# Optimization experiments

Measured on AMD Instinct MI355X. Metric: run time of the kernel, lower is better.

## Reference

```python
import jax, jax.numpy as jnp
import numpy as np
import math

B, N, C = 8, 4096, 768
H = 12
DH = C // H
M = 256
LN_EPS = 1e-5


def setup_inputs() -> dict:
    key = jax.random.key(0)
    ks = jax.random.split(key, 7)
    x = jax.random.normal(ks[0], (B, N, C), dtype=jnp.float32)
    # torch Linear weight [out,in]; store transposed for y = x @ W
    W_qkv = jax.random.normal(ks[1], (C, 3 * C), dtype=jnp.float32) * (1.0 / math.sqrt(C))
    W_proj = jax.random.normal(ks[2], (C, C), dtype=jnp.float32) * (1.0 / math.sqrt(C))
    b_proj = jnp.zeros((C,), dtype=jnp.float32)
    gamma = jnp.ones((C,), dtype=jnp.float32)
    beta = jnp.zeros((C,), dtype=jnp.float32)
    random_features = jax.random.normal(ks[3], (M, DH), dtype=jnp.float32) / math.sqrt(DH)
    return {"x": x, "W_qkv": W_qkv, "W_proj": W_proj, "b_proj": b_proj,
            "gamma": gamma, "beta": beta, "random_features": random_features}


def _phi(t, random_features):
    # t: [B, H, N, DH] -> [B, H, N, M]; phi(x) = exp(w·x - ||x||^2/2) / sqrt(M)
    norm_sq = 0.5 * jnp.sum(t * t, axis=-1, keepdims=True)
    proj = jnp.einsum('bhnd,md->bhnm', t, random_features)
    return jnp.exp(proj - norm_sq) * (1.0 / math.sqrt(M))


def reference(x, W_qkv, W_proj, b_proj, gamma, beta, random_features):
    b, n, c = x.shape
    qkv = (x @ W_qkv).reshape(b, n, 3, H, DH)
    qkv = jnp.transpose(qkv, (2, 0, 3, 1, 4))  # [3, B, H, N, DH]
    q, k, v = qkv[0], qkv[1], qkv[2]

    q_p = _phi(q, random_features)  # [B,H,N,M]
    k_p = _phi(k, random_features)  # [B,H,N,M]

    kv = jnp.einsum('bhnm,bhnd->bhmd', k_p, v)       # [B,H,M,DH]
    out = jnp.einsum('bhnm,bhmd->bhnd', q_p, kv)     # [B,H,N,DH]

    k_sum = jnp.sum(k_p, axis=2)                      # [B,H,M]
    normalizer = jnp.einsum('bhnm,bhm->bhn', q_p, k_sum)[..., None]
    out = out / (normalizer + 1e-6)

    x_attn = jnp.transpose(out, (0, 2, 1, 3)).reshape(b, n, c)
    x_attn = x_attn @ W_proj + b_proj
    # dropout is identity in eval / p=0

    y = x + x_attn
    mu = jnp.mean(y, axis=-1, keepdims=True)
    var = jnp.mean(jnp.square(y - mu), axis=-1, keepdims=True)
    return (y - mu) * jax.lax.rsqrt(var + LN_EPS) * gamma + beta
```

## Files before the change

kernel.cpp:

```cpp
#include <hip/hip_runtime.h>
#include <hip/hip_fp16.h>


#define LOG2E 1.44269504088896340736f

typedef _Float16 half8 __attribute__((ext_vector_type(8)));
typedef _Float16 half4_t __attribute__((ext_vector_type(4)));
typedef _Float16 half2_t __attribute__((ext_vector_type(2)));
typedef float f32x4 __attribute__((ext_vector_type(4)));

#if __has_builtin(__builtin_amdgcn_fdot2)
#define FDOT2(a, b, c) __builtin_amdgcn_fdot2((a), (b), (c), false)
#else
#define FDOT2(a, b, c) \
  ((float)(a)[0] * (float)(b)[0] + ((float)(a)[1] * (float)(b)[1] + (c)))
#endif

static __device__ __forceinline__ half2_t pk2(float a, float b) {
#if __has_builtin(__builtin_amdgcn_cvt_pkrtz)
  return __builtin_bit_cast(half2_t, __builtin_amdgcn_cvt_pkrtz(a, b));
#else
  half2_t r; r[0] = (_Float16)a; r[1] = (_Float16)b; return r;
#endif
}

__device__ __forceinline__ void glds16(const _Float16* g, _Float16* s) {
  __builtin_amdgcn_global_load_lds(
      (const __attribute__((address_space(1))) void*)g,
      (__attribute__((address_space(3))) unsigned int*)s,
      16, 0, 0);
}


__global__ __launch_bounds__(256)
void prep(const float* __restrict__ x, const float* __restrict__ Wqkv,
          const float* __restrict__ Wproj, const float* __restrict__ rfm,
          _Float16* __restrict__ x_h, _Float16* __restrict__ wqkvT,
          _Float16* __restrict__ wprojT, _Float16* __restrict__ rfh) {
  __shared__ _Float16 T[64][72];
  const int bid = blockIdx.x;
  if (bid < 12288) {
    long i = ((long)bid * 256 + threadIdx.x) * 8;
    float4 v0 = *(const float4*)(x + i);
    float4 v1 = *(const float4*)(x + i + 4);
    half8 h;
    h[0] = (_Float16)v0.x; h[1] = (_Float16)v0.y; h[2] = (_Float16)v0.z; h[3] = (_Float16)v0.w;
    h[4] = (_Float16)v1.x; h[5] = (_Float16)v1.y; h[6] = (_Float16)v1.z; h[7] = (_Float16)v1.w;
    *(half8*)(x_h + i) = h;
    return;
  }
  int tb = bid - 12288;
  if (tb < 576) {
    const float* src; _Float16* dst; int Csrc, r0, c0;
    if (tb < 432) {
      r0 = (tb / 36) * 64; c0 = (tb % 36) * 64; src = Wqkv; dst = wqkvT; Csrc = 2304;
    } else {
      int t2 = tb - 432;
      r0 = (t2 / 12) * 64; c0 = (t2 % 12) * 64; src = Wproj; dst = wprojT; Csrc = 768;
    }
    const int ri = threadIdx.x >> 4;
    const int ci = (threadIdx.x & 15) * 4;
#pragma unroll
    for (int rr = 0; rr < 4; ++rr) {
      float4 v = *(const float4*)(src + (long)(r0 + ri * 4 + rr) * Csrc + c0 + ci);
      T[ci + 0][ri * 4 + rr] = (_Float16)v.x;
      T[ci + 1][ri * 4 + rr] = (_Float16)v.y;
      T[ci + 2][ri * 4 + rr] = (_Float16)v.z;
      T[ci + 3][ri * 4 + rr] = (_Float16)v.w;
    }
    __syncthreads();
    const int wi = threadIdx.x >> 3;
    const int wj = (threadIdx.x & 7) * 8;
#pragma unroll
    for (int ww = 0; ww < 2; ++ww) {
      const int row = wi * 2 + ww;
      half8 h = *(const half8*)(&T[row][wj]);
      *(half8*)(dst + (long)(c0 + row) * 768 + r0 + wj) = h;
    }
  } else {
    int idx = (tb - 576) * 256 + threadIdx.x;
    if (idx < 16384) rfh[idx] = (_Float16)rfm[idx];
  }
}


__device__ __forceinline__ void stage_unit(const _Float16* __restrict__ G, int grow0,
                                           int kcol, _Float16* lds, int w, int l) {
#pragma unroll
  for (int j = 0; j < 2; ++j) {
    const int ci = w + j * 8;
    const int row = ci * 8 + (l >> 3);
    const int col8 = (l & 7) ^ (row & 7);
    glds16(G + (long)(grow0 + row) * 768 + kcol + col8 * 8, lds + ci * 512);
  }
}

static __device__ __forceinline__ half8 ldsw(const _Float16* buf, int r, int sl) {
  return *(const half8*)(buf + r * 64 + ((sl ^ (r & 7)) << 3));
}

__global__ __launch_bounds__(512)
void gemm_qkv(const _Float16* __restrict__ W, const _Float16* __restrict__ X,
              _Float16* __restrict__ qh, _Float16* __restrict__ kh,
              _Float16* __restrict__ vT,
              float* __restrict__ nsqLq, float* __restrict__ nsqLk) {
  __shared__ __align__(16) _Float16 SMEM[65536];
  _Float16* As = SMEM;
  _Float16* Bs = SMEM + 32768;
  const int tid = threadIdx.x;
  const int w = tid >> 6, l = tid & 63;
  const int lr = l & 15, kg = l >> 4;
  const int wr = w >> 2, wc = w & 3;

  const int bid = blockIdx.x;
  const int wg = (bid & 7) * 144 + (bid >> 3);
  const int m0 = (wg % 9) * 256;
  const int n0 = (wg / 9) * 256;

  stage_unit(W, m0,       0,  As,         w, l);
  stage_unit(W, m0 + 128, 0,  As + 8192,  w, l);
  stage_unit(X, n0,       0,  Bs,         w, l);
  stage_unit(X, n0 + 128, 0,  Bs + 8192,  w, l);
  stage_unit(W, m0,       64, As + 16384, w, l);
  stage_unit(X, n0,       64, Bs + 16384, w, l);
  stage_unit(X, n0 + 128, 64, Bs + 24576, w, l);
  asm volatile("s_waitcnt vmcnt(6)" ::: "memory");
  __builtin_amdgcn_s_barrier();

  f32x4 acc[8][4];
#pragma unroll
  for (int t = 0; t < 8; ++t)
#pragma unroll
    for (int u = 0; u < 4; ++u) acc[t][u] = (f32x4){0.f, 0.f, 0.f, 0.f};

  for (int kt = 0; kt < 12; ++kt) {
    const int c = kt & 1, o = c ^ 1;
    const _Float16* Ac = As + c * 16384;
    const _Float16* Bc = Bs + c * 16384;
    half8 a0[4][2], a1[4][2], b0[2][2], b1[2][2];

#pragma unroll
    for (int i = 0; i < 4; ++i) {
      const int r = wr * 16 + i * 32 + lr;
      a0[i][0] = ldsw(Ac, r, kg);
      a0[i][1] = ldsw(Ac, r, 4 + kg);
    }
#pragma unroll
    for (int j = 0; j < 2; ++j) {
      const int r = wc * 16 + j * 64 + lr;
      b0[j][0] = ldsw(Bc, r, kg);
      b0[j][1] = ldsw(Bc, r, 4 + kg);
    }
#pragma unroll
    for (int j = 0; j < 2; ++j) {
      const int r = 128 + wc * 16 + j * 64 + lr;
      b1[j][0] = ldsw(Bc, r, kg);
      b1[j][1] = ldsw(Bc, r, 4 + kg);
    }
#pragma unroll
    for (int i = 0; i < 4; ++i) {
      const int r = 128 + wr * 16 + i * 32 + lr;
      a1[i][0] = ldsw(Ac, r, kg);
      a1[i][1] = ldsw(Ac, r, 4 + kg);
    }
    if (kt + 1 < 12)
      stage_unit(W, m0 + 128, (kt + 1) * 64, As + o * 16384 + 8192, w, l);

    __builtin_amdgcn_s_setprio(1);
#pragma unroll
    for (int ks = 0; ks < 2; ++ks)
#pragma unroll
      for (int i = 0; i < 4; ++i)
#pragma unroll
        for (int j = 0; j < 2; ++j)
          acc[i][j] = __builtin_amdgcn_mfma_f32_16x16x32_f16(a0[i][ks], b0[j][ks],
                                                             acc[i][j], 0, 0, 0);
#pragma unroll
    for (int ks = 0; ks < 2; ++ks)
#pragma unroll
      for (int i = 0; i < 4; ++i)
#pragma unroll
        for (int j = 0; j < 2; ++j)
          acc[i][2 + j] = __builtin_amdgcn_mfma_f32_16x16x32_f16(a0[i][ks], b1[j][ks],
                                                                 acc[i][2 + j], 0, 0, 0);
#pragma unroll
    for (int ks = 0; ks < 2; ++ks)
#pragma unroll
      for (int i = 0; i < 4; ++i)
#pragma unroll
        for (int j = 0; j < 2; ++j)
          acc[4 + i][2 + j] = __builtin_amdgcn_mfma_f32_16x16x32_f16(a1[i][ks], b1[j][ks],
                                                                     acc[4 + i][2 + j], 0, 0, 0);
#pragma unroll
    for (int ks = 0; ks < 2; ++ks)
#pragma unroll
      for (int i = 0; i < 4; ++i)
#pragma unroll
        for (int j = 0; j < 2; ++j)
          acc[4 + i][j] = __builtin_amdgcn_mfma_f32_16x16x32_f16(a1[i][ks], b0[j][ks],
                                                                 acc[4 + i][j], 0, 0, 0);
    __builtin_amdgcn_s_setprio(0);

    __builtin_amdgcn_s_barrier();
    if (kt + 2 < 12) {
      stage_unit(W, m0, (kt + 2) * 64, As + c * 16384, w, l);
      stage_unit(X, n0, (kt + 2) * 64, Bs + c * 16384, w, l);
      stage_unit(X, n0 + 128, (kt + 2) * 64, Bs + c * 16384 + 8192, w, l);
    }
    if (kt < 10)
      asm volatile("s_waitcnt vmcnt(6)" ::: "memory");
    else
      asm volatile("s_waitcnt vmcnt(0)" ::: "memory");
    __builtin_amdgcn_s_barrier();
  }

  const int which = (m0 >= 1536) ? 2 : ((m0 >= 768) ? 1 : 0);
  const int hbase = (m0 - which * 768) >> 6;
  const int b_ = n0 >> 12;
  const int nb = n0 & 4095;

  if (which < 2) {
    _Float16* dst = which ? kh : qh;
    float* nd = which ? nsqLk : nsqLq;
#pragma unroll
    for (int t = 0; t < 8; ++t) {
      const int m_ = wr * 16 + t * 32 + kg * 4;
#pragma unroll
      for (int u = 0; u < 4; ++u) {
        const int n_ = wc * 16 + u * 64 + lr;
        half2_t h01 = pk2(acc[t][u][0], acc[t][u][1]);
        half2_t h23 = pk2(acc[t][u][2], acc[t][u][3]);
        half4_t p4; p4[0] = h01[0]; p4[1] = h01[1]; p4[2] = h23[0]; p4[3] = h23[1];
        *(half4_t*)((char*)SMEM + n_ * 512 + (((m_ >> 3) ^ (n_ & 7)) << 4) +
                    (m_ & 4) * 2) = p4;
      }
    }
    __syncthreads();
    const int h2 = w >> 1;
    const int jj = l & 7;
    const long bhout = (long)(b_ * 12 + hbase + h2);
#pragma unroll
    for (int i = 0; i < 16; ++i) {
      const int n_ = (w & 1) * 128 + i * 8 + (l >> 3);
      const int phys = (h2 * 8 + jj) ^ (n_ & 7);
      half8 v = *(const half8*)((const char*)SMEM + n_ * 512 + phys * 16);
      *(half8*)(dst + (bhout * 4096 + nb + n_) * 64 + jj * 8) = v;
      float s = 0.f;
#pragma unroll
      for (int e = 0; e < 8; ++e) { float f = (float)v[e]; s += f * f; }
      s += __shfl_xor(s, 1);
      s += __shfl_xor(s, 2);
      s += __shfl_xor(s, 4);
      if (jj == 0) nd[bhout * 4096 + nb + n_] = 0.5f * s * LOG2E + 4.0f;
    }
  } else {
#pragma unroll
    for (int t = 0; t < 8; ++t) {
#pragma unroll
      for (int u = 0; u < 4; ++u) {
        const int n_ = wc * 16 + u * 64 + lr;
#pragma unroll
        for (int r = 0; r < 4; ++r) {
          const int m_ = wr * 16 + t * 32 + kg * 4 + r;
          *(_Float16*)((char*)SMEM + m_ * 512 + ((((n_ >> 3)) ^ (m_ & 7)) << 4) +
                       (n_ & 7) * 2) = (_Float16)acc[t][u][r];
        }
      }
    }
    __syncthreads();
#pragma unroll
    for (int i = 0; i < 16; ++i) {
      const int m_ = w * 32 + i * 2 + (l >> 5);
      const int c = l & 31;
      half8 v = *(const half8*)((const char*)SMEM + m_ * 512 + ((c ^ (m_ & 7)) << 4));
      const int h2 = m_ >> 6, d = m_ & 63;
      *(half8*)(vT + ((long)(b_ * 12 + hbase + h2) * 64 + d) * 4096 + nb + c * 8) = v;
    }
  }
}


__global__ __launch_bounds__(512)
void proj_ln(const _Float16* __restrict__ A, const _Float16* __restrict__ BT,
             const float* __restrict__ bias, const float* __restrict__ xres,
             const float* __restrict__ gamma, const float* __restrict__ beta,
             float* __restrict__ y) {
  __shared__ __align__(16) _Float16 Asm[64 * 768];
  __shared__ __align__(16) float lnS[64][8];
  __shared__ __align__(16) float lnQ[64][8];
  const int tid = threadIdx.x;
  const int w = tid >> 6, l = tid & 63;
  const int lr = l & 15, kg = l >> 4;
  const int m0 = blockIdx.x * 64;
  const int ncol0 = w * 96;

#pragma unroll
  for (int i = 0; i < 12; ++i) {
    const int sg = i * 512 + tid;
    const int row = sg / 96;
    const int p = sg - row * 96;
    glds16(A + (long)(m0 + row) * 768 + ((p ^ (row & 7)) << 3), Asm + sg * 8);
  }
  asm volatile("s_waitcnt vmcnt(0)" ::: "memory");
  __builtin_amdgcn_s_barrier();

  f32x4 acc[4][6];
#pragma unroll
  for (int mf = 0; mf < 4; ++mf)
#pragma unroll
    for (int nf = 0; nf < 6; ++nf) acc[mf][nf] = (f32x4){0.f, 0.f, 0.f, 0.f};

#pragma unroll 2
  for (int kc = 0; kc < 12; ++kc) {
    half8 bf[6][2];
#pragma unroll
    for (int nf = 0; nf < 6; ++nf)
#pragma unroll
      for (int ks = 0; ks < 2; ++ks)
        bf[nf][ks] = *(const half8*)(BT + (long)(ncol0 + nf * 16 + lr) * 768 +
                                     kc * 64 + ks * 32 + kg * 8);
    half8 af[4][2];
#pragma unroll
    for (int mf = 0; mf < 4; ++mf) {
      const int r = mf * 16 + lr;
#pragma unroll
      for (int ks = 0; ks < 2; ++ks)
        af[mf][ks] = *(const half8*)(Asm + r * 768 +
                                     (((kc * 8 + ks * 4 + kg) ^ (lr & 7)) << 3));
    }
#pragma unroll
    for (int ks = 0; ks < 2; ++ks)
#pragma unroll
      for (int mf = 0; mf < 4; ++mf)
#pragma unroll
        for (int nf = 0; nf < 6; ++nf)
          acc[mf][nf] = __builtin_amdgcn_mfma_f32_16x16x32_f16(af[mf][ks], bf[nf][ks],
                                                               acc[mf][nf], 0, 0, 0);
  }

  float bv[6], gv[6], betv[6];
#pragma unroll
  for (int nf = 0; nf < 6; ++nf) {
    const int col = ncol0 + nf * 16 + lr;
    bv[nf] = bias[col]; gv[nf] = gamma[col]; betv[nf] = beta[col];
  }
#pragma unroll
  for (int mf = 0; mf < 4; ++mf)
#pragma unroll
    for (int r = 0; r < 4; ++r) {
      const int row = mf * 16 + kg * 4 + r;
#pragma unroll
      for (int nf = 0; nf < 6; ++nf)
        acc[mf][nf][r] += bv[nf] + xres[(long)(m0 + row) * 768 + ncol0 + nf * 16 + lr];
    }
#pragma unroll
  for (int mf = 0; mf < 4; ++mf)
#pragma unroll
    for (int r = 0; r < 4; ++r) {
      float s = 0.f, q = 0.f;
#pragma unroll
      for (int nf = 0; nf < 6; ++nf) {
        const float v = acc[mf][nf][r];
        s += v; q += v * v;
      }
      s += __shfl_xor(s, 1); q += __shfl_xor(q, 1);
      s += __shfl_xor(s, 2); q += __shfl_xor(q, 2);
      s += __shfl_xor(s, 4); q += __shfl_xor(q, 4);
      s += __shfl_xor(s, 8); q += __shfl_xor(q, 8);
      if (lr == 0) {
        const int row = mf * 16 + kg * 4 + r;
        lnS[row][w] = s; lnQ[row][w] = q;
      }
    }
  __syncthreads();
#pragma unroll
  for (int mf = 0; mf < 4; ++mf)
#pragma unroll
    for (int r = 0; r < 4; ++r) {
      const int row = mf * 16 + kg * 4 + r;
      f32x4 s0 = *(const f32x4*)&lnS[row][0];
      f32x4 s1 = *(const f32x4*)&lnS[row][4];
      f32x4 q0 = *(const f32x4*)&lnQ[row][0];
      f32x4 q1 = *(const f32x4*)&lnQ[row][4];
      const float s = s0[0] + s0[1] + s0[2] + s0[3] + s1[0] + s1[1] + s1[2] + s1[3];
      const float q = q0[0] + q0[1] + q0[2] + q0[3] + q1[0] + q1[1] + q1[2] + q1[3];
      const float mu = s * (1.f / 768.f);
      const float var = q * (1.f / 768.f) - mu * mu;
      const float rstd = rsqrtf(var + 1e-5f);
#pragma unroll
      for (int nf = 0; nf < 6; ++nf)
        y[(long)(m0 + row) * 768 + ncol0 + nf * 16 + lr] =
            (acc[mf][nf][r] - mu) * rstd * gv[nf] + betv[nf];
    }
}


__global__ __launch_bounds__(256)
void kv_fused(const _Float16* __restrict__ kh, const _Float16* __restrict__ vT,
              const _Float16* __restrict__ rfh, const float* __restrict__ nsqLk,
              _Float16* __restrict__ kvpart, float* __restrict__ kspart) {
  __shared__ __align__(16) _Float16 P[256 * 72];
  const int chunk = blockIdx.x, bh = blockIdx.y;
  const int tid = threadIdx.x, w = tid >> 6, l = tid & 63;
  const int lr = l & 15, kg = l >> 4;
  const long khbase = (long)bh * 4096 * 64;
  const long vtbase = (long)bh * 64 * 4096;
  const half2_t ONES = {(_Float16)1.f, (_Float16)1.f};

  half8 rf[4][2];
#pragma unroll
  for (int u = 0; u < 4; ++u)
#pragma unroll
    for (int ks = 0; ks < 2; ++ks)
      rf[u][ks] = *(const half8*)(rfh + (w * 64 + u * 16 + lr) * 64 + ks * 32 + kg * 8);

  f32x4 kvacc[4][4];
#pragma unroll
  for (int mt = 0; mt < 4; ++mt)
#pragma unroll
    for (int dt = 0; dt < 4; ++dt) kvacc[mt][dt] = (f32x4){0.f, 0.f, 0.f, 0.f};
  float ksacc[4] = {0.f, 0.f, 0.f, 0.f};

  for (int t8 = 0; t8 < 8; ++t8) {
    const int nt = chunk * 512 + t8 * 64;

    half8 af[4][2];
#pragma unroll
    for (int tt = 0; tt < 4; ++tt)
#pragma unroll
      for (int ks = 0; ks < 2; ++ks)
        af[tt][ks] = *(const half8*)(kh + khbase + (long)(nt + tt * 16 + lr) * 64 +
                                     ks * 32 + kg * 8);

    f32x4 sacc[4][4];
#pragma unroll
    for (int tt = 0; tt < 4; ++tt)
#pragma unroll
      for (int u = 0; u < 4; ++u) sacc[tt][u] = (f32x4){0.f, 0.f, 0.f, 0.f};
#pragma unroll
    for (int ks = 0; ks < 2; ++ks)
#pragma unroll
      for (int tt = 0; tt < 4; ++tt)
#pragma unroll
        for (int u = 0; u < 4; ++u)
          sacc[tt][u] = __builtin_amdgcn_mfma_f32_16x16x32_f16(af[tt][ks], rf[u][ks],
                                                               sacc[tt][u], 0, 0, 0);
    float4 nsq4[4];
#pragma unroll
    for (int tt = 0; tt < 4; ++tt)
      nsq4[tt] = *(const float4*)(nsqLk + (long)bh * 4096 + nt + tt * 16 + kg * 4);
#pragma unroll
    for (int tt = 0; tt < 4; ++tt)
#pragma unroll
      for (int u = 0; u < 4; ++u) {
        float e0 = exp2f(sacc[tt][u][0] * LOG2E - nsq4[tt].x);
        float e1 = exp2f(sacc[tt][u][1] * LOG2E - nsq4[tt].y);
        float e2 = exp2f(sacc[tt][u][2] * LOG2E - nsq4[tt].z);
        float e3 = exp2f(sacc[tt][u][3] * LOG2E - nsq4[tt].w);
        half2_t h01 = pk2(e0, e1), h23 = pk2(e2, e3);
        half4_t p4; p4[0] = h01[0]; p4[1] = h01[1]; p4[2] = h23[0]; p4[3] = h23[1];
        *(half4_t*)(P + (w * 64 + u * 16 + lr) * 72 + tt * 16 + kg * 4) = p4;
      }

#pragma unroll
    for (int ks = 0; ks < 2; ++ks) {
      half8 pa[4], bv[4];
#pragma unroll
      for (int mt = 0; mt < 4; ++mt)
        pa[mt] = *(const half8*)(P + (w * 64 + mt * 16 + lr) * 72 + ks * 32 + kg * 8);
#pragma unroll
      for (int dt = 0; dt < 4; ++dt)
        bv[dt] = *(const half8*)(vT + vtbase + (long)(dt * 16 + lr) * 4096 + nt +
                                 ks * 32 + kg * 8);
#pragma unroll
      for (int mt = 0; mt < 4; ++mt)
#pragma unroll
        for (int dt = 0; dt < 4; ++dt)
          kvacc[mt][dt] = __builtin_amdgcn_mfma_f32_16x16x32_f16(pa[mt], bv[dt],
                                                                 kvacc[mt][dt], 0, 0, 0);
#pragma unroll
      for (int mt = 0; mt < 4; ++mt) {
        const half2_t* pp = (const half2_t*)&pa[mt];
#pragma unroll
        for (int p = 0; p < 4; ++p) ksacc[mt] = FDOT2(pp[p], ONES, ksacc[mt]);
      }
    }
  }

#pragma unroll
  for (int mt = 0; mt < 4; ++mt) {
    float v = ksacc[mt];
    v += __shfl_xor(v, 16);
    v += __shfl_xor(v, 32);
    if (l < 16) kspart[((bh * 8 + chunk) << 8) + w * 64 + mt * 16 + l] = v;
  }
#pragma unroll
  for (int mt = 0; mt < 4; ++mt)
#pragma unroll
    for (int dt = 0; dt < 4; ++dt)
#pragma unroll
      for (int r = 0; r < 4; ++r)
        kvpart[(((long)(bh * 8 + chunk) * 256) + w * 64 + mt * 16 + kg * 4 + r) * 64 +
               dt * 16 + lr] = (_Float16)kvacc[mt][dt][r];
}


__global__ __launch_bounds__(256)
void reduce_all(const _Float16* __restrict__ kvpart, const float* __restrict__ kspart,
                _Float16* __restrict__ kvT, _Float16* __restrict__ ksumh) {
  if (blockIdx.x < 6144) {
    long i = (long)blockIdx.x * 256 + threadIdx.x;
    const int bh = (int)(i >> 14);
    const int rem = (int)(i & 16383);
    const int m = rem >> 6, d = rem & 63;
    float s = 0.f;
#pragma unroll
    for (int c = 0; c < 8; ++c)
      s += (float)kvpart[(((long)bh * 8 + c) * 256 + m) * 64 + d];
    kvT[(long)bh * 16384 + d * 256 + m] = (_Float16)s;
  } else {
    int i = (blockIdx.x - 6144) * 256 + threadIdx.x;
    int bh = i >> 8, m = i & 255;
    float s = 0.f;
#pragma unroll
    for (int c = 0; c < 8; ++c) s += kspart[((bh * 8 + c) << 8) + m];
    ksumh[i] = (_Float16)s;
  }
}


__global__ __launch_bounds__(256)
void attn_fused(const _Float16* __restrict__ qh, const _Float16* __restrict__ rfh,
                const float* __restrict__ nsqLq, const _Float16* __restrict__ kvT,
                const _Float16* __restrict__ ksumh, _Float16* __restrict__ attn) {
  __shared__ __align__(16) _Float16 KV[64 * 264];
  __shared__ __align__(16) _Float16 KS[256];
  __shared__ __align__(16) _Float16 P[64 * 264];
  __shared__ __align__(16) float NS[64];
  const int chunk = blockIdx.x, bh = blockIdx.y;
  const int b = bh / 12, h = bh % 12;
  const int tid = threadIdx.x, w = tid >> 6, l = tid & 63;
  const int lr = l & 15, kg = l >> 4;

  {
    const int d = tid >> 2, mb = (tid & 3) * 64;
#pragma unroll
    for (int j = 0; j < 8; ++j)
      *(half8*)(KV + d * 264 + mb + j * 8) =
          *(const half8*)(kvT + (long)bh * 16384 + d * 256 + mb + j * 8);
    if (tid < 32) *(half8*)(KS + tid * 8) = *(const half8*)(ksumh + bh * 256 + tid * 8);
  }

  half8 rf[4][2];
#pragma unroll
  for (int mt = 0; mt < 4; ++mt)
#pragma unroll
    for (int ks = 0; ks < 2; ++ks)
      rf[mt][ks] = *(const half8*)(rfh + (w * 64 + mt * 16 + lr) * 64 + ks * 32 + kg * 8);

  for (int t8 = 0; t8 < 4; ++t8) {
    const int nt = chunk * 256 + t8 * 64;
    __syncthreads();

    half8 bq[4][2];
#pragma unroll
    for (int tt = 0; tt < 4; ++tt)
#pragma unroll
      for (int ks = 0; ks < 2; ++ks)
        bq[tt][ks] = *(const half8*)(qh + ((long)bh * 4096 + nt + tt * 16 + lr) * 64 +
                                     ks * 32 + kg * 8);

    f32x4 sacc[4][4];
#pragma unroll
    for (int mt = 0; mt < 4; ++mt)
#pragma unroll
      for (int tt = 0; tt < 4; ++tt) sacc[mt][tt] = (f32x4){0.f, 0.f, 0.f, 0.f};
#pragma unroll
    for (int ks = 0; ks < 2; ++ks)
#pragma unroll
      for (int mt = 0; mt < 4; ++mt)
#pragma unroll
        for (int tt = 0; tt < 4; ++tt)
          sacc[mt][tt] = __builtin_amdgcn_mfma_f32_16x16x32_f16(rf[mt][ks], bq[tt][ks],
                                                                sacc[mt][tt], 0, 0, 0);
    float nsqv[4];
#pragma unroll
    for (int tt = 0; tt < 4; ++tt)
      nsqv[tt] = nsqLq[(long)bh * 4096 + nt + tt * 16 + lr];
#pragma unroll
    for (int mt = 0; mt < 4; ++mt)
#pragma unroll
      for (int tt = 0; tt < 4; ++tt) {
        float e0 = exp2f(sacc[mt][tt][0] * LOG2E - nsqv[tt]);
        float e1 = exp2f(sacc[mt][tt][1] * LOG2E - nsqv[tt]);
        float e2 = exp2f(sacc[mt][tt][2] * LOG2E - nsqv[tt]);
        float e3 = exp2f(sacc[mt][tt][3] * LOG2E - nsqv[tt]);
        half2_t h01 = pk2(e0, e1), h23 = pk2(e2, e3);
        half4_t p4; p4[0] = h01[0]; p4[1] = h01[1]; p4[2] = h23[0]; p4[3] = h23[1];
        *(half4_t*)(P + (tt * 16 + lr) * 264 + w * 64 + mt * 16 + kg * 4) = p4;
      }
    __syncthreads();

    f32x4 oacc[4];
#pragma unroll
    for (int u = 0; u < 4; ++u) oacc[u] = (f32x4){0.f, 0.f, 0.f, 0.f};
    float nacc = 0.f;
#pragma unroll
    for (int ks = 0; ks < 8; ++ks) {
      half8 ap = *(const half8*)(P + (w * 16 + lr) * 264 + ks * 32 + kg * 8);
      half8 kv8 = *(const half8*)(KS + ks * 32 + kg * 8);
      const half2_t* a2 = (const half2_t*)&ap;
      const half2_t* k2 = (const half2_t*)&kv8;
#pragma unroll
      for (int p = 0; p < 4; ++p) nacc = FDOT2(a2[p], k2[p], nacc);
#pragma unroll
      for (int u = 0; u < 4; ++u) {
        half8 bkv = *(const half8*)(KV + (u * 16 + lr) * 264 + ks * 32 + kg * 8);
        oacc[u] = __builtin_amdgcn_mfma_f32_16x16x32_f16(ap, bkv, oacc[u], 0, 0, 0);
      }
    }
    nacc += __shfl_xor(nacc, 16);
    nacc += __shfl_xor(nacc, 32);
    if (l < 16) NS[w * 16 + l] = nacc;
    f32x4 n4 = *(const f32x4*)(NS + w * 16 + kg * 4);
    float inv[4];
#pragma unroll
    for (int r = 0; r < 4; ++r) inv[r] = 1.f / (n4[r] + 1e-6f);
#pragma unroll
    for (int u = 0; u < 4; ++u)
#pragma unroll
      for (int r = 0; r < 4; ++r)
        attn[((long)b * 4096 + nt + w * 16 + kg * 4 + r) * 768 + h * 64 + u * 16 + lr] =
            (_Float16)(oacc[u][r] * inv[r]);
  }
}


extern "C" void kernel_launch(void* const* d_in, const int* in_sizes, int n_in,
                              void* d_out, int out_size, void* d_ws, size_t ws_size,
                              hipStream_t stream) {
  const float* x = (const float*)d_in[0];
  const float* Wqkv = (const float*)d_in[1];
  const float* Wproj = (const float*)d_in[2];
  const float* bproj = (const float*)d_in[3];
  const float* gamma = (const float*)d_in[4];
  const float* beta = (const float*)d_in[5];
  const float* rfm = (const float*)d_in[6];

  char* ws = (char*)d_ws;
  size_t off = 0;
  auto alloc = [&](size_t bytes) -> void* {
    void* p = ws + off;
    off += (bytes + 255) & ~(size_t)255;
    return p;
  };
  char* regionA = (char*)alloc(50331648ULL);
  _Float16* x_h = (_Float16*)regionA;
  _Float16* kvpart = (_Float16*)regionA;
  _Float16* attn = (_Float16*)regionA;

  _Float16* wqkvT = (_Float16*)alloc(1769472ULL * 2);
  _Float16* wprojT = (_Float16*)alloc(589824ULL * 2);
  _Float16* rfh = (_Float16*)alloc(16384ULL * 2);
  _Float16* qh = (_Float16*)alloc(25165824ULL * 2);
  _Float16* kh = (_Float16*)alloc(25165824ULL * 2);
  _Float16* vT = (_Float16*)alloc(25165824ULL * 2);
  float* nsqLq = (float*)alloc(393216ULL * 4);
  float* nsqLk = (float*)alloc(393216ULL * 4);
  float* kspart = (float*)alloc(96ULL * 8 * 256 * 4);
  _Float16* kvT = (_Float16*)alloc(96ULL * 16384 * 2);
  _Float16* ksumh = (_Float16*)alloc(96ULL * 256 * 2);

  float* y = (float*)d_out;

  prep<<<12928, 256, 0, stream>>>(x, Wqkv, Wproj, rfm, x_h, wqkvT, wprojT, rfh);
  gemm_qkv<<<1152, 512, 0, stream>>>(wqkvT, x_h, qh, kh, vT, nsqLq, nsqLk);
  kv_fused<<<dim3(8, 96), 256, 0, stream>>>(kh, vT, rfh, nsqLk, kvpart, kspart);
  reduce_all<<<6240, 256, 0, stream>>>(kvpart, kspart, kvT, ksumh);
  attn_fused<<<dim3(16, 96), 256, 0, stream>>>(qh, rfh, nsqLq, kvT, ksumh, attn);
  proj_ln<<<512, 512, 0, stream>>>(attn, wprojT, bproj, x, gamma, beta, y);
}
```

Baseline: 578.1 us.

## Shrink QKV GEMM tile to 128x128 with triple-buffered BK=32 pipeline

The QKV projection GEMM moves from 256x256 tiles with 512 threads and double-buffered K=64 stages to 128x128 tiles with 256 threads and a three-stage ring of K=32 buffers. It uses a new swizzled LDS layout and a lighter epilogue. The goal is higher occupancy, since LDS use drops from 128KB to 48KB per block, and a grid of 4608 blocks for better load balance across CUs. The cost is lower arithmetic intensity per tile, so more global and LDS traffic per FLOP, and more barriers per unit of K.

```diff
diff --git a/kernel.cpp b/kernel.cpp
--- a/kernel.cpp
+++ b/kernel.cpp
@@ -84,134 +84,80 @@
 }
 
 
-__device__ __forceinline__ void stage_unit(const _Float16* __restrict__ G, int grow0,
-                                           int kcol, _Float16* lds, int w, int l) {
+__device__ __forceinline__ void stage32(const _Float16* __restrict__ G, int grow0,
+                                        int kcol, _Float16* lds, int w, int l) {
 #pragma unroll
   for (int j = 0; j < 2; ++j) {
-    const int ci = w + j * 8;
-    const int row = ci * 8 + (l >> 3);
-    const int col8 = (l & 7) ^ (row & 7);
-    glds16(G + (long)(grow0 + row) * 768 + kcol + col8 * 8, lds + ci * 512);
-  }
-}
-
-static __device__ __forceinline__ half8 ldsw(const _Float16* buf, int r, int sl) {
-  return *(const half8*)(buf + r * 64 + ((sl ^ (r & 7)) << 3));
-}
-
-__global__ __launch_bounds__(512)
+    const int ci = w + j * 4;
+    const int p = ci * 8 + (l >> 3);
+    const int tmp = (l & 7) ^ (p & 7);
+    const int r = 2 * p + (tmp >> 2);
+    const int kc = tmp & 3;
+    glds16(G + (long)(grow0 + r) * 768 + kcol + kc * 8, lds + ci * 512);
+  }
+}
+
+static __device__ __forceinline__ half8 ld32(const _Float16* buf, int m, int kg) {
+  return *(const half8*)((const char*)buf + (m >> 1) * 128 +
+                         (((kg + (m & 1) * 4) ^ ((m >> 1) & 7)) << 4));
+}
+
+__global__ __launch_bounds__(256)
 void gemm_qkv(const _Float16* __restrict__ W, const _Float16* __restrict__ X,
               _Float16* __restrict__ qh, _Float16* __restrict__ kh,
               _Float16* __restrict__ vT,
               float* __restrict__ nsqLq, float* __restrict__ nsqLk) {
-  __shared__ __align__(16) _Float16 SMEM[65536];
-  _Float16* As = SMEM;
-  _Float16* Bs = SMEM + 32768;
+  __shared__ __align__(16) _Float16 SMEM[24576];
   const int tid = threadIdx.x;
   const int w = tid >> 6, l = tid & 63;
   const int lr = l & 15, kg = l >> 4;
-  const int wr = w >> 2, wc = w & 3;
+  const int wm = (w >> 1) * 64, wn = (w & 1) * 64;
 
   const int bid = blockIdx.x;
-  const int wg = (bid & 7) * 144 + (bid >> 3);
-  const int m0 = (wg % 9) * 256;
-  const int n0 = (wg / 9) * 256;
-
-  stage_unit(W, m0,       0,  As,         w, l);
-  stage_unit(W, m0 + 128, 0,  As + 8192,  w, l);
-  stage_unit(X, n0,       0,  Bs,         w, l);
-  stage_unit(X, n0 + 128, 0,  Bs + 8192,  w, l);
-  stage_unit(W, m0,       64, As + 16384, w, l);
-  stage_unit(X, n0,       64, Bs + 16384, w, l);
-  stage_unit(X, n0 + 128, 64, Bs + 24576, w, l);
-  asm volatile("s_waitcnt vmcnt(6)" ::: "memory");
+  const int wg = (bid & 7) * 576 + (bid >> 3);
+  const int m0 = (wg % 18) * 128;
+  const int n0 = (wg / 18) * 128;
+
+  stage32(W, m0, 0, SMEM, w, l);
+  stage32(X, n0, 0, SMEM + 4096, w, l);
+  stage32(W, m0, 32, SMEM + 8192, w, l);
+  stage32(X, n0, 32, SMEM + 8192 + 4096, w, l);
+  asm volatile("s_waitcnt vmcnt(4)" ::: "memory");
   __builtin_amdgcn_s_barrier();
 
-  f32x4 acc[8][4];
-#pragma unroll
-  for (int t = 0; t < 8; ++t)
+  f32x4 acc[4][4];
+#pragma unroll
+  for (int t = 0; t < 4; ++t)
 #pragma unroll
     for (int u = 0; u < 4; ++u) acc[t][u] = (f32x4){0.f, 0.f, 0.f, 0.f};
 
-  for (int kt = 0; kt < 12; ++kt) {
-    const int c = kt & 1, o = c ^ 1;
-    const _Float16* Ac = As + c * 16384;
-    const _Float16* Bc = Bs + c * 16384;
-    half8 a0[4][2], a1[4][2], b0[2][2], b1[2][2];
-
-#pragma unroll
-    for (int i = 0; i < 4; ++i) {
-      const int r = wr * 16 + i * 32 + lr;
-      a0[i][0] = ldsw(Ac, r, kg);
-      a0[i][1] = ldsw(Ac, r, 4 + kg);
-    }
-#pragma unroll
-    for (int j = 0; j < 2; ++j) {
-      const int r = wc * 16 + j * 64 + lr;
-      b0[j][0] = ldsw(Bc, r, kg);
-      b0[j][1] = ldsw(Bc, r, 4 + kg);
-    }
-#pragma unroll
-    for (int j = 0; j < 2; ++j) {
-      const int r = 128 + wc * 16 + j * 64 + lr;
-      b1[j][0] = ldsw(Bc, r, kg);
-      b1[j][1] = ldsw(Bc, r, 4 + kg);
-    }
-#pragma unroll
-    for (int i = 0; i < 4; ++i) {
-      const int r = 128 + wr * 16 + i * 32 + lr;
-      a1[i][0] = ldsw(Ac, r, kg);
-      a1[i][1] = ldsw(Ac, r, 4 + kg);
-    }
-    if (kt + 1 < 12)
-      stage_unit(W, m0 + 128, (kt + 1) * 64, As + o * 16384 + 8192, w, l);
-
+  int s = 0, s2 = 2;
+  for (int kt = 0; kt < 24; ++kt) {
+    const _Float16* Ab = SMEM + s * 8192;
+    const _Float16* Bb = Ab + 4096;
+    half8 af[4], bf[4];
+#pragma unroll
+    for (int t = 0; t < 4; ++t) af[t] = ld32(Ab, wm + t * 16 + lr, kg);
+#pragma unroll
+    for (int u = 0; u < 4; ++u) bf[u] = ld32(Bb, wn + u * 16 + lr, kg);
+    if (kt + 2 < 24) {
+      stage32(W, m0, (kt + 2) * 32, SMEM + s2 * 8192, w, l);
+      stage32(X, n0, (kt + 2) * 32, SMEM + s2 * 8192 + 4096, w, l);
+    }
     __builtin_amdgcn_s_setprio(1);
 #pragma unroll
-    for (int ks = 0; ks < 2; ++ks)
-#pragma unroll
-      for (int i = 0; i < 4; ++i)
-#pragma unroll
-        for (int j = 0; j < 2; ++j)
-          acc[i][j] = __builtin_amdgcn_mfma_f32_16x16x32_f16(a0[i][ks], b0[j][ks],
-                                                             acc[i][j], 0, 0, 0);
-#pragma unroll
-    for (int ks = 0; ks < 2; ++ks)
-#pragma unroll
-      for (int i = 0; i < 4; ++i)
-#pragma unroll
-        for (int j = 0; j < 2; ++j)
-          acc[i][2 + j] = __builtin_amdgcn_mfma_f32_16x16x32_f16(a0[i][ks], b1[j][ks],
-                                                                 acc[i][2 + j], 0, 0, 0);
-#pragma unroll
-    for (int ks = 0; ks < 2; ++ks)
-#pragma unroll
-      for (int i = 0; i < 4; ++i)
-#pragma unroll
-        for (int j = 0; j < 2; ++j)
-          acc[4 + i][2 + j] = __builtin_amdgcn_mfma_f32_16x16x32_f16(a1[i][ks], b1[j][ks],
-                                                                     acc[4 + i][2 + j], 0, 0, 0);
-#pragma unroll
-    for (int ks = 0; ks < 2; ++ks)
-#pragma unroll
-      for (int i = 0; i < 4; ++i)
-#pragma unroll
-        for (int j = 0; j < 2; ++j)
-          acc[4 + i][j] = __builtin_amdgcn_mfma_f32_16x16x32_f16(a1[i][ks], b0[j][ks],
-                                                                 acc[4 + i][j], 0, 0, 0);
+    for (int t = 0; t < 4; ++t)
+#pragma unroll
+      for (int u = 0; u < 4; ++u)
+        acc[t][u] = __builtin_amdgcn_mfma_f32_16x16x32_f16(af[t], bf[u], acc[t][u], 0, 0, 0);
     __builtin_amdgcn_s_setprio(0);
-
-    __builtin_amdgcn_s_barrier();
-    if (kt + 2 < 12) {
-      stage_unit(W, m0, (kt + 2) * 64, As + c * 16384, w, l);
-      stage_unit(X, n0, (kt + 2) * 64, Bs + c * 16384, w, l);
-      stage_unit(X, n0 + 128, (kt + 2) * 64, Bs + c * 16384 + 8192, w, l);
-    }
-    if (kt < 10)
-      asm volatile("s_waitcnt vmcnt(6)" ::: "memory");
+    if (kt < 22)
+      asm volatile("s_waitcnt vmcnt(4)" ::: "memory");
     else
       asm volatile("s_waitcnt vmcnt(0)" ::: "memory");
     __builtin_amdgcn_s_barrier();
+    s = (s == 2) ? 0 : s + 1;
+    s2 = (s2 == 2) ? 0 : s2 + 1;
   }
 
   const int which = (m0 >= 1536) ? 2 : ((m0 >= 768) ? 1 : 0);
@@ -223,58 +169,59 @@
     _Float16* dst = which ? kh : qh;
     float* nd = which ? nsqLk : nsqLq;
 #pragma unroll
-    for (int t = 0; t < 8; ++t) {
-      const int m_ = wr * 16 + t * 32 + kg * 4;
+    for (int t = 0; t < 4; ++t) {
+      const int m_ = wm + t * 16 + kg * 4;
 #pragma unroll
       for (int u = 0; u < 4; ++u) {
-        const int n_ = wc * 16 + u * 64 + lr;
+        const int n_ = wn + u * 16 + lr;
         half2_t h01 = pk2(acc[t][u][0], acc[t][u][1]);
         half2_t h23 = pk2(acc[t][u][2], acc[t][u][3]);
         half4_t p4; p4[0] = h01[0]; p4[1] = h01[1]; p4[2] = h23[0]; p4[3] = h23[1];
-        *(half4_t*)((char*)SMEM + n_ * 512 + (((m_ >> 3) ^ (n_ & 7)) << 4) +
+        *(half4_t*)((char*)SMEM + n_ * 256 + (((m_ >> 3) ^ (n_ & 7)) << 4) +
                     (m_ & 4) * 2) = p4;
       }
     }
     __syncthreads();
-    const int h2 = w >> 1;
+    const int h2 = w & 1;
     const int jj = l & 7;
     const long bhout = (long)(b_ * 12 + hbase + h2);
 #pragma unroll
-    for (int i = 0; i < 16; ++i) {
-      const int n_ = (w & 1) * 128 + i * 8 + (l >> 3);
+    for (int i = 0; i < 8; ++i) {
+      const int n_ = (w >> 1) * 64 + i * 8 + (l >> 3);
       const int phys = (h2 * 8 + jj) ^ (n_ & 7);
-      half8 v = *(const half8*)((const char*)SMEM + n_ * 512 + phys * 16);
+      half8 v = *(const half8*)((const char*)SMEM + n_ * 256 + phys * 16);
       *(half8*)(dst + (bhout * 4096 + nb + n_) * 64 + jj * 8) = v;
-      float s = 0.f;
-#pragma unroll
-      for (int e = 0; e < 8; ++e) { float f = (float)v[e]; s += f * f; }
-      s += __shfl_xor(s, 1);
-      s += __shfl_xor(s, 2);
-      s += __shfl_xor(s, 4);
-      if (jj == 0) nd[bhout * 4096 + nb + n_] = 0.5f * s * LOG2E + 4.0f;
+      float sq = 0.f;
+#pragma unroll
+      for (int e = 0; e < 8; ++e) { float f = (float)v[e]; sq += f * f; }
+      sq += __shfl_xor(sq, 1);
+      sq += __shfl_xor(sq, 2);
+      sq += __shfl_xor(sq, 4);
+      if (jj == 0) nd[bhout * 4096 + nb + n_] = 0.5f * sq * LOG2E + 4.0f;
     }
   } else {
 #pragma unroll
-    for (int t = 0; t < 8; ++t) {
+    for (int t = 0; t < 4; ++t) {
 #pragma unroll
       for (int u = 0; u < 4; ++u) {
-        const int n_ = wc * 16 + u * 64 + lr;
+        const int n_ = wn + u * 16 + lr;
 #pragma unroll
         for (int r = 0; r < 4; ++r) {
-          const int m_ = wr * 16 + t * 32 + kg * 4 + r;
-          *(_Float16*)((char*)SMEM + m_ * 512 + ((((n_ >> 3)) ^ (m_ & 7)) << 4) +
+          const int m_ = wm + t * 16 + kg * 4 + r;
+          *(_Float16*)((char*)SMEM + m_ * 256 + (((n_ >> 3) ^ (m_ & 7)) << 4) +
                        (n_ & 7) * 2) = (_Float16)acc[t][u][r];
         }
       }
     }
     __syncthreads();
-#pragma unroll
-    for (int i = 0; i < 16; ++i) {
-      const int m_ = w * 32 + i * 2 + (l >> 5);
-      const int c = l & 31;
-      half8 v = *(const half8*)((const char*)SMEM + m_ * 512 + ((c ^ (m_ & 7)) << 4));
+    const int c16 = tid & 15;
+#pragma unroll
+    for (int i = 0; i < 8; ++i) {
+      const int m_ = i * 16 + (tid >> 4);
+      const int phys = c16 ^ (m_ & 7);
+      half8 v = *(const half8*)((const char*)SMEM + m_ * 256 + phys * 16);
       const int h2 = m_ >> 6, d = m_ & 63;
-      *(half8*)(vT + ((long)(b_ * 12 + hbase + h2) * 64 + d) * 4096 + nb + c * 8) = v;
+      *(half8*)(vT + ((long)(b_ * 12 + hbase + h2) * 64 + d) * 4096 + nb + c16 * 8) = v;
     }
   }
 }
@@ -674,7 +621,7 @@
   float* y = (float*)d_out;
 
   prep<<<12928, 256, 0, stream>>>(x, Wqkv, Wproj, rfm, x_h, wqkvT, wprojT, rfh);
-  gemm_qkv<<<1152, 512, 0, stream>>>(wqkvT, x_h, qh, kh, vT, nsqLq, nsqLk);
+  gemm_qkv<<<4608, 256, 0, stream>>>(wqkvT, x_h, qh, kh, vT, nsqLq, nsqLk);
   kv_fused<<<dim3(8, 96), 256, 0, stream>>>(kh, vT, rfh, nsqLk, kvpart, kspart);
   reduce_all<<<6240, 256, 0, stream>>>(kvpart, kspart, kvT, ksumh);
   attn_fused<<<dim3(16, 96), 256, 0, stream>>>(qh, rfh, nsqLq, kvT, ksumh, attn);
```

Result: no change. 582.7 us (+0.8%).
